# Performance work log

Measured on AMD Instinct MI355X. Metric: run time of the kernel, lower is better.

## Reference

```python
import jax, jax.numpy as jnp
import numpy as np
import math

B = 1048576
BG_RES = 512
NUM_LEVELS = 2
POWER = 4
MIPNOISE = 0.5
INIT_VAL = -2.0


def cube_face_uv(v):
    # v: [N,3] direction vectors. OpenGL cubemap face convention
    # (faces: 0:+x 1:-x 2:+y 3:-y 4:+z 5:-z), as used by nvdiffrast 'cube'.
    x, y, z = v[:, 0], v[:, 1], v[:, 2]
    ax, ay, az = jnp.abs(x), jnp.abs(y), jnp.abs(z)
    is_x = (ax >= ay) & (ax >= az)
    is_y = (~is_x) & (ay >= az)
    face = jnp.where(is_x, jnp.where(x >= 0, 0, 1),
                     jnp.where(is_y, jnp.where(y >= 0, 2, 3),
                               jnp.where(z >= 0, 4, 5))).astype(jnp.int32)
    ma = jnp.where(is_x, ax, jnp.where(is_y, ay, az))
    sc = jnp.where(is_x, jnp.where(x >= 0, -z, z),
                   jnp.where(is_y, x, jnp.where(z >= 0, x, -x)))
    tc = jnp.where(is_x, -y, jnp.where(is_y, jnp.where(y >= 0, z, -z), -y))
    u = 0.5 * (sc / ma + 1.0)
    t = 0.5 * (tc / ma + 1.0)
    return face, u, t


def build_pyramid(tex):
    # tex: [6,R,R,3] -> list of 2x2 box-filtered mips down to 1x1 (nvdiffrast style)
    levels = [tex]
    t = tex
    while t.shape[1] > 1:
        R = t.shape[1]
        t = t.reshape(6, R // 2, 2, R // 2, 2, 3).mean(axis=(2, 4))
        levels.append(t)
    return levels


def bilinear(tex, face, u, v):
    # tex: [6,R,R,3]; face/u/v: [N]. Clamp-to-edge bilinear per selected face.
    R = tex.shape[1]
    x = u * R - 0.5
    y = v * R - 0.5
    x0f = jnp.floor(x); y0f = jnp.floor(y)
    fx = (x - x0f)[:, None]; fy = (y - y0f)[:, None]
    x0 = jnp.clip(x0f.astype(jnp.int32), 0, R - 1)
    y0 = jnp.clip(y0f.astype(jnp.int32), 0, R - 1)
    x1 = jnp.clip(x0f.astype(jnp.int32) + 1, 0, R - 1)
    y1 = jnp.clip(y0f.astype(jnp.int32) + 1, 0, R - 1)
    flat = tex.reshape(6 * R * R, 3)
    base = face * (R * R)
    g00 = flat[base + y0 * R + x0]
    g01 = flat[base + y0 * R + x1]
    g10 = flat[base + y1 * R + x0]
    g11 = flat[base + y1 * R + x1]
    return ((1 - fx) * (1 - fy) * g00 + fx * (1 - fy) * g01 +
            (1 - fx) * fy * g10 + fx * fy * g11)


def sample_cubemap(tex6, face, u, v, mip):
    # trilinear: bilinear in two adjacent mips, lerp by fractional mip level
    levels = build_pyramid(tex6)
    lmax = float(len(levels) - 1)
    m = jnp.clip(mip, 0.0, lmax)
    out = jnp.zeros((face.shape[0], 3), tex6.dtype)
    for l, t in enumerate(levels):
        wl = jnp.clip(1.0 - jnp.abs(m - l), 0.0, 1.0)  # (1-f)/f trilinear weights
        out = out + wl[:, None] * bilinear(t, face, u, v)
    return out


def setup_inputs() -> dict:
    key = jax.random.key(0)
    k1, k2, k3, k4, k5 = jax.random.split(key, 5)
    viewdirs = jax.random.normal(k1, (B, 3), dtype=jnp.float32)
    viewdirs = viewdirs / jnp.linalg.norm(viewdirs, axis=-1, keepdims=True)
    saSample = jax.random.normal(k2, (B,), dtype=jnp.float32)
    noise_u = jax.random.uniform(k3, (B,), dtype=jnp.float32)
    # parameters (init_val*ones/(num_levels-i) in torch; perturbed for nontrivial grads)
    bg_mat0 = (INIT_VAL * jnp.ones((1, 6, 128, 128, 3), jnp.float32)
               + 0.1 * jax.random.normal(k4, (1, 6, 128, 128, 3), jnp.float32))
    bg_mat1 = (INIT_VAL / 2.0 * jnp.ones((1, 6, 512, 512, 3), jnp.float32)
               + 0.1 * jax.random.normal(k5, (1, 6, 512, 512, 3), jnp.float32))
    return {
        "viewdirs": viewdirs,
        "saSample": saSample,
        "noise_u": noise_u,
        "bg_mat0": bg_mat0,
        "bg_mat1": bg_mat1,
        "brightness": jnp.asarray(0.0, jnp.float32),
        "mul": jnp.asarray(1.0, jnp.float32),
        "mipbias": jnp.asarray(0.5, jnp.float32),
    }


def reference(viewdirs, saSample, noise_u, bg_mat0, bg_mat1, brightness, mul, mipbias):
    h = w = BG_RES  # from bg_mats[-1]
    # sa2mip
    distortion = 1.0 / jnp.max(jnp.abs(viewdirs), axis=-1)  # 1/||u||_inf
    saTexel = distortion / h / w
    miplevel = ((saSample - jnp.log(saTexel)) / math.log(POWER) / 2.0
                + mipbias + MIPNOISE * noise_u)
    miplevel = jnp.maximum(miplevel, 0.0)

    face, u, t = cube_face_uv(viewdirs)
    sumemb = sample_cubemap(bg_mat0[0], face, u, t, miplevel)  # mip 1 (128)
    sumemb = sumemb + sample_cubemap(bg_mat1[0], face, u, t, miplevel)  # mip 0 (512)

    # activation == 'identity' branch: exp(x).clip(0.01, 1000)
    img = jnp.clip(jnp.exp(jnp.clip(brightness, -1.0, 2.0) + mul * sumemb), 0.01, 1000.0)
    return img
```

## Files before the change

kernel.cpp:

```cpp
#include <hip/hip_runtime.h>
#include <hip/hip_bf16.h>
#include <math.h>


#define NPYR1_4 524286

__device__ __constant__ int OFFS0[7] = {0, 24576, 30720, 32256, 32640, 32736, 32760};
__device__ __constant__ int OFFS1[9] = {0, 393216, 491520, 516096, 522240,
                                        523776, 524160, 524256, 524280};
static const int H_OFFS0[7] = {0, 24576, 30720, 32256, 32640, 32736, 32760};
static const int H_OFFS1[9] = {0, 393216, 491520, 516096, 522240,
                               523776, 524160, 524256, 524280};

struct PyrArgs {
    const void* src;
    float4* dst[5];
    int R;
    int tpf;
    int T;
    int nlev;
    int rgba;
};

__global__ __launch_bounds__(256) void pyr_kernel(PyrArgs a0, PyrArgs a1, int split) {
    __shared__ float4 A[32 * 32];
    __shared__ float4 Bb[16 * 16];

    PyrArgs a = (blockIdx.x < (unsigned)split) ? a0 : a1;
    int bid = (blockIdx.x < (unsigned)split) ? blockIdx.x : blockIdx.x - split;

    const int tpf = a.tpf;
    const int face = bid / (tpf * tpf);
    const int tif = bid - face * tpf * tpf;
    const int ty = tif / tpf, tx = tif - (tif / tpf) * tpf;
    const int T = a.T, R = a.R;
    const int tid = threadIdx.x;
    const int baseY = ty * T, baseX = tx * T;

    const int total = T * T;
    if (a.rgba) {
        const float4* src = (const float4*)a.src;
        for (int idx = tid; idx < total; idx += 256) {
            int r = idx / T, c = idx - (idx / T) * T;
            A[r * T + c] = src[(size_t)(face * R + baseY + r) * R + baseX + c];
        }
    } else {
        const float* src = (const float*)a.src;
        for (int idx = tid; idx < total; idx += 256) {
            int r = idx / T, c = idx - (idx / T) * T;
            const float* p = src + ((size_t)(face * R + baseY + r) * R + baseX + c) * 3;
            A[r * T + c] = make_float4(p[0], p[1], p[2], 0.f);
        }
    }
    __syncthreads();

    float4* cur = A;
    float4* nxt = Bb;
    int curT = T;
    for (int l = 0; l < a.nlev; ++l) {
        const int nT = curT >> 1;
        const int Rg = R >> (l + 1);
        const int tb = T >> (l + 1);
        float4* dst = a.dst[l];
        const int n = nT * nT;
        for (int idx = tid; idx < n; idx += 256) {
            int ly = idx / nT, lx = idx - (idx / nT) * nT;
            float4 q00 = cur[(2 * ly) * curT + 2 * lx];
            float4 q01 = cur[(2 * ly) * curT + 2 * lx + 1];
            float4 q10 = cur[(2 * ly + 1) * curT + 2 * lx];
            float4 q11 = cur[(2 * ly + 1) * curT + 2 * lx + 1];
            float4 s = make_float4(0.25f * (q00.x + q01.x + q10.x + q11.x),
                                   0.25f * (q00.y + q01.y + q10.y + q11.y),
                                   0.25f * (q00.z + q01.z + q10.z + q11.z), 0.f);
            nxt[ly * nT + lx] = s;
            dst[(size_t)(face * Rg + ty * tb + ly) * Rg + tx * tb + lx] = s;
        }
        __syncthreads();
        float4* tmp = cur; cur = nxt; nxt = tmp;
        curT = nT;
    }
}

__device__ __forceinline__ void bilin4(const float4* __restrict__ tex, int R,
                                       int face, float u, float v, float o[3]) {
    float xf = u * (float)R - 0.5f;
    float yf = v * (float)R - 0.5f;
    float x0f = floorf(xf), y0f = floorf(yf);
    float fx = xf - x0f, fy = yf - y0f;
    int xi = (int)x0f, yi = (int)y0f;
    int x0 = min(max(xi, 0), R - 1);
    int x1 = min(max(xi + 1, 0), R - 1);
    int y0 = min(max(yi, 0), R - 1);
    int y1 = min(max(yi + 1, 0), R - 1);
    const float4* base = tex + (size_t)face * R * R;
    float4 p00 = base[y0 * R + x0];
    float4 p01 = base[y0 * R + x1];
    float4 p10 = base[y1 * R + x0];
    float4 p11 = base[y1 * R + x1];
    float w00 = (1.f - fx) * (1.f - fy);
    float w01 = fx * (1.f - fy);
    float w10 = (1.f - fx) * fy;
    float w11 = fx * fy;
    o[0] = w00 * p00.x + w01 * p01.x + w10 * p10.x + w11 * p11.x;
    o[1] = w00 * p00.y + w01 * p01.y + w10 * p10.y + w11 * p11.y;
    o[2] = w00 * p00.z + w01 * p01.z + w10 * p10.z + w11 * p11.z;
}

__device__ __forceinline__ void bilin3(const float* __restrict__ tex, int R,
                                       int face, float u, float v, float o[3]) {
    float xf = u * (float)R - 0.5f;
    float yf = v * (float)R - 0.5f;
    float x0f = floorf(xf), y0f = floorf(yf);
    float fx = xf - x0f, fy = yf - y0f;
    int xi = (int)x0f, yi = (int)y0f;
    int x0 = min(max(xi, 0), R - 1);
    int x1 = min(max(xi + 1, 0), R - 1);
    int y0 = min(max(yi, 0), R - 1);
    int y1 = min(max(yi + 1, 0), R - 1);
    const float* base = tex + (size_t)face * R * R * 3;
    const float* p00 = base + (y0 * R + x0) * 3;
    const float* p01 = base + (y0 * R + x1) * 3;
    const float* p10 = base + (y1 * R + x0) * 3;
    const float* p11 = base + (y1 * R + x1) * 3;
    float w00 = (1.f - fx) * (1.f - fy);
    float w01 = fx * (1.f - fy);
    float w10 = (1.f - fx) * fy;
    float w11 = fx * fy;
#pragma unroll
    for (int c = 0; c < 3; ++c)
        o[c] = w00 * p00[c] + w01 * p01[c] + w10 * p10[c] + w11 * p11[c];
}

__device__ __forceinline__ void sample_pyr(const float* __restrict__ base_tex,
                                           const float4* __restrict__ pyr,
                                           const int* offs, int lmax, int R0,
                                           int face, float u, float v, float mip,
                                           float o[3]) {
    float m = fminf(fmaxf(mip, 0.f), (float)lmax);
    float l0f = floorf(m);
    int l0 = (int)l0f;
    float f = m - l0f;
    float c0[3];
    if (l0 == 0)
        bilin3(base_tex, R0, face, u, v, c0);
    else
        bilin4(pyr + offs[l0 - 1], R0 >> l0, face, u, v, c0);
    if (f > 0.f && l0 < lmax) {
        float c1[3];
        bilin4(pyr + offs[l0], R0 >> (l0 + 1), face, u, v, c1);
        float w0 = 1.f - f;
#pragma unroll
        for (int c = 0; c < 3; ++c) o[c] = w0 * c0[c] + f * c1[c];
    } else {
#pragma unroll
        for (int c = 0; c < 3; ++c) o[c] = c0[c];
    }
}

__global__ __launch_bounds__(256) void sample_kernel(
    const float* __restrict__ vd, const float* __restrict__ sa,
    const float* __restrict__ nu, const float* __restrict__ tex0,
    const float* __restrict__ tex1, const float* __restrict__ sb,
    const float* __restrict__ sm, const float* __restrict__ smb,
    const float4* __restrict__ pyr0, const float4* __restrict__ pyr1,
    float* __restrict__ out, int n) {
    int i = blockIdx.x * 256 + threadIdx.x;
    if (i >= n) return;

    float x = vd[3 * i + 0];
    float y = vd[3 * i + 1];
    float z = vd[3 * i + 2];
    float ax = fabsf(x), ay = fabsf(y), az = fabsf(z);

    bool is_x = (ax >= ay) && (ax >= az);
    bool is_y = (!is_x) && (ay >= az);

    int face;
    float ma, sc, tc;
    if (is_x) {
        face = (x >= 0.f) ? 0 : 1;
        ma = ax;
        sc = (x >= 0.f) ? -z : z;
        tc = -y;
    } else if (is_y) {
        face = (y >= 0.f) ? 2 : 3;
        ma = ay;
        sc = x;
        tc = (y >= 0.f) ? z : -z;
    } else {
        face = (z >= 0.f) ? 4 : 5;
        ma = az;
        sc = (z >= 0.f) ? x : -x;
        tc = -y;
    }
    float u = 0.5f * (sc / ma + 1.f);
    float t = 0.5f * (tc / ma + 1.f);

    float distortion = 1.f / ma;
    float saTexel = distortion / 512.f / 512.f;
    float mip = (sa[i] - logf(saTexel)) / 1.3862943611198906f / 2.0f +
                smb[0] + 0.5f * nu[i];
    mip = fmaxf(mip, 0.f);

    float s0[3], s1[3];
    sample_pyr(tex0, pyr0, OFFS0, 7, 128, face, u, t, mip, s0);
    sample_pyr(tex1, pyr1, OFFS1, 9, 512, face, u, t, mip, s1);

    float b = fminf(fmaxf(sb[0], -1.f), 2.f);
    float mul = sm[0];
#pragma unroll
    for (int c = 0; c < 3; ++c) {
        float e = expf(b + mul * (s0[c] + s1[c]));
        out[3 * i + c] = fminf(fmaxf(e, 0.01f), 1000.f);
    }
}

extern "C" void kernel_launch(void* const* d_in, const int* in_sizes, int n_in,
                              void* d_out, int out_size, void* d_ws, size_t ws_size,
                              hipStream_t stream) {
    const float* vd = (const float*)d_in[0];
    const float* sa = (const float*)d_in[1];
    const float* nu = (const float*)d_in[2];
    const float* tex0 = (const float*)d_in[3];
    const float* tex1 = (const float*)d_in[4];
    const float* br = (const float*)d_in[5];
    const float* mu = (const float*)d_in[6];
    const float* mb = (const float*)d_in[7];
    float* out = (float*)d_out;

    float4* pyr1 = (float4*)d_ws;
    float4* pyr0 = pyr1 + NPYR1_4;

    const int B = in_sizes[1];

    PyrArgs a0{}, a1{};
    a0.src = tex1; a0.R = 512; a0.tpf = 16; a0.T = 32; a0.nlev = 5; a0.rgba = 0;
    for (int l = 0; l < 5; ++l) a0.dst[l] = pyr1 + H_OFFS1[l];
    a1.src = tex0; a1.R = 128; a1.tpf = 4; a1.T = 32; a1.nlev = 5; a1.rgba = 0;
    for (int l = 0; l < 5; ++l) a1.dst[l] = pyr0 + H_OFFS0[l];
    int split1 = 6 * 16 * 16;
    int grid1 = split1 + 6 * 4 * 4;
    hipLaunchKernelGGL(pyr_kernel, dim3(grid1), dim3(256), 0, stream, a0, a1, split1);

    PyrArgs b0{}, b1{};
    b0.src = pyr1 + H_OFFS1[4]; b0.R = 16; b0.tpf = 1; b0.T = 16; b0.nlev = 4; b0.rgba = 1;
    for (int l = 0; l < 4; ++l) b0.dst[l] = pyr1 + H_OFFS1[5 + l];
    b1.src = pyr0 + H_OFFS0[4]; b1.R = 4; b1.tpf = 1; b1.T = 4; b1.nlev = 2; b1.rgba = 1;
    for (int l = 0; l < 2; ++l) b1.dst[l] = pyr0 + H_OFFS0[5 + l];
    hipLaunchKernelGGL(pyr_kernel, dim3(12), dim3(256), 0, stream, b0, b1, 6);

    int grid = (B + 255) / 256;
    hipLaunchKernelGGL(sample_kernel, dim3(grid), dim3(256), 0, stream,
                       vd, sa, nu, tex0, tex1, br, mu, mb, pyr0, pyr1, out, B);
}
```

Before: 137.4 us.

## Fuse coarse mip levels into sampling kernel via shared-memory pyramid

Removes the second tiny pyramid launch. Each block of a persistent grid-stride sampling kernel (512 blocks) now loads the 16x16 and smaller mip levels into LDS, reduces them to 1x1 there, and samples the coarse levels from LDS instead of global memory. This cuts a serialized launch and global traffic for the coarse taps. The cost is about 64KB of LDS per block, which limits occupancy, plus redundant per-block reduction work.

```diff
diff --git a/kernel.cpp b/kernel.cpp
--- a/kernel.cpp
+++ b/kernel.cpp
@@ -11,6 +11,8 @@
 static const int H_OFFS0[7] = {0, 24576, 30720, 32256, 32640, 32736, 32760};
 static const int H_OFFS1[9] = {0, 393216, 491520, 516096, 522240,
                                523776, 524160, 524256, 524280};
+
+__device__ __constant__ int LOFF[5] = {0, 1536, 1920, 2016, 2040};
 
 struct PyrArgs {
     const void* src;
@@ -19,7 +21,6 @@
     int tpf;
     int T;
     int nlev;
-    int rgba;
 };
 
 __global__ __launch_bounds__(256) void pyr_kernel(PyrArgs a0, PyrArgs a1, int split) {
@@ -38,19 +39,11 @@
     const int baseY = ty * T, baseX = tx * T;
 
     const int total = T * T;
-    if (a.rgba) {
-        const float4* src = (const float4*)a.src;
-        for (int idx = tid; idx < total; idx += 256) {
-            int r = idx / T, c = idx - (idx / T) * T;
-            A[r * T + c] = src[(size_t)(face * R + baseY + r) * R + baseX + c];
-        }
-    } else {
-        const float* src = (const float*)a.src;
-        for (int idx = tid; idx < total; idx += 256) {
-            int r = idx / T, c = idx - (idx / T) * T;
-            const float* p = src + ((size_t)(face * R + baseY + r) * R + baseX + c) * 3;
-            A[r * T + c] = make_float4(p[0], p[1], p[2], 0.f);
-        }
+    const float* src = (const float*)a.src;
+    for (int idx = tid; idx < total; idx += 256) {
+        int r = idx / T, c = idx - (idx / T) * T;
+        const float* p = src + ((size_t)(face * R + baseY + r) * R + baseX + c) * 3;
+        A[r * T + c] = make_float4(p[0], p[1], p[2], 0.f);
     }
     __syncthreads();
 
@@ -81,26 +74,32 @@
     }
 }
 
-__device__ __forceinline__ void bilin4(const float4* __restrict__ tex, int R,
-                                       int face, float u, float v, float o[3]) {
+
+__device__ __forceinline__ void wuv(int R, float u, float v, int& x0, int& x1,
+                                    int& y0, int& y1, float& fx, float& fy) {
     float xf = u * (float)R - 0.5f;
     float yf = v * (float)R - 0.5f;
     float x0f = floorf(xf), y0f = floorf(yf);
-    float fx = xf - x0f, fy = yf - y0f;
+    fx = xf - x0f;
+    fy = yf - y0f;
     int xi = (int)x0f, yi = (int)y0f;
-    int x0 = min(max(xi, 0), R - 1);
-    int x1 = min(max(xi + 1, 0), R - 1);
-    int y0 = min(max(yi, 0), R - 1);
-    int y1 = min(max(yi + 1, 0), R - 1);
+    x0 = min(max(xi, 0), R - 1);
+    x1 = min(max(xi + 1, 0), R - 1);
+    y0 = min(max(yi, 0), R - 1);
+    y1 = min(max(yi + 1, 0), R - 1);
+}
+
+__device__ __forceinline__ void bilin4(const float4* __restrict__ tex, int R,
+                                       int face, float u, float v, float o[3]) {
+    int x0, x1, y0, y1; float fx, fy;
+    wuv(R, u, v, x0, x1, y0, y1, fx, fy);
     const float4* base = tex + (size_t)face * R * R;
     float4 p00 = base[y0 * R + x0];
     float4 p01 = base[y0 * R + x1];
     float4 p10 = base[y1 * R + x0];
     float4 p11 = base[y1 * R + x1];
-    float w00 = (1.f - fx) * (1.f - fy);
-    float w01 = fx * (1.f - fy);
-    float w10 = (1.f - fx) * fy;
-    float w11 = fx * fy;
+    float w00 = (1.f - fx) * (1.f - fy), w01 = fx * (1.f - fy);
+    float w10 = (1.f - fx) * fy, w11 = fx * fy;
     o[0] = w00 * p00.x + w01 * p01.x + w10 * p10.x + w11 * p11.x;
     o[1] = w00 * p00.y + w01 * p01.y + w10 * p10.y + w11 * p11.y;
     o[2] = w00 * p00.z + w01 * p01.z + w10 * p10.z + w11 * p11.z;
@@ -108,52 +107,71 @@
 
 __device__ __forceinline__ void bilin3(const float* __restrict__ tex, int R,
                                        int face, float u, float v, float o[3]) {
-    float xf = u * (float)R - 0.5f;
-    float yf = v * (float)R - 0.5f;
-    float x0f = floorf(xf), y0f = floorf(yf);
-    float fx = xf - x0f, fy = yf - y0f;
-    int xi = (int)x0f, yi = (int)y0f;
-    int x0 = min(max(xi, 0), R - 1);
-    int x1 = min(max(xi + 1, 0), R - 1);
-    int y0 = min(max(yi, 0), R - 1);
-    int y1 = min(max(yi + 1, 0), R - 1);
+    int x0, x1, y0, y1; float fx, fy;
+    wuv(R, u, v, x0, x1, y0, y1, fx, fy);
     const float* base = tex + (size_t)face * R * R * 3;
     const float* p00 = base + (y0 * R + x0) * 3;
     const float* p01 = base + (y0 * R + x1) * 3;
     const float* p10 = base + (y1 * R + x0) * 3;
     const float* p11 = base + (y1 * R + x1) * 3;
-    float w00 = (1.f - fx) * (1.f - fy);
-    float w01 = fx * (1.f - fy);
-    float w10 = (1.f - fx) * fy;
-    float w11 = fx * fy;
+    float w00 = (1.f - fx) * (1.f - fy), w01 = fx * (1.f - fy);
+    float w10 = (1.f - fx) * fy, w11 = fx * fy;
 #pragma unroll
     for (int c = 0; c < 3; ++c)
         o[c] = w00 * p00[c] + w01 * p01[c] + w10 * p10[c] + w11 * p11[c];
 }
 
-__device__ __forceinline__ void sample_pyr(const float* __restrict__ base_tex,
-                                           const float4* __restrict__ pyr,
-                                           const int* offs, int lmax, int R0,
-                                           int face, float u, float v, float mip,
-                                           float o[3]) {
-    float m = fminf(fmaxf(mip, 0.f), (float)lmax);
-    float l0f = floorf(m);
-    int l0 = (int)l0f;
-    float f = m - l0f;
-    float c0[3];
-    if (l0 == 0)
-        bilin3(base_tex, R0, face, u, v, c0);
-    else
-        bilin4(pyr + offs[l0 - 1], R0 >> l0, face, u, v, c0);
-    if (f > 0.f && l0 < lmax) {
-        float c1[3];
-        bilin4(pyr + offs[l0], R0 >> (l0 + 1), face, u, v, c1);
-        float w0 = 1.f - f;
-#pragma unroll
-        for (int c = 0; c < 3; ++c) o[c] = w0 * c0[c] + f * c1[c];
-    } else {
-#pragma unroll
-        for (int c = 0; c < 3; ++c) o[c] = c0[c];
+__device__ __forceinline__ void bilinL(const float4* __restrict__ L, int lb, int R,
+                                       int face, float u, float v, float o[3]) {
+    int x0, x1, y0, y1; float fx, fy;
+    wuv(R, u, v, x0, x1, y0, y1, fx, fy);
+    const float4* base = L + lb + face * R * R;
+    float4 p00 = base[y0 * R + x0];
+    float4 p01 = base[y0 * R + x1];
+    float4 p10 = base[y1 * R + x0];
+    float4 p11 = base[y1 * R + x1];
+    float w00 = (1.f - fx) * (1.f - fy), w01 = fx * (1.f - fy);
+    float w10 = (1.f - fx) * fy, w11 = fx * fy;
+    o[0] = w00 * p00.x + w01 * p01.x + w10 * p10.x + w11 * p11.x;
+    o[1] = w00 * p00.y + w01 * p01.y + w10 * p10.y + w11 * p11.y;
+    o[2] = w00 * p00.z + w01 * p01.z + w10 * p10.z + w11 * p11.z;
+}
+
+__device__ __forceinline__ void tap1(const float4* __restrict__ L,
+                                     const float* __restrict__ tex1,
+                                     const float4* __restrict__ pyr1, int l,
+                                     int face, float u, float v, float o[3]) {
+    if (l >= 5)      bilinL(L, LOFF[l - 5], 16 >> (l - 5), face, u, v, o);
+    else if (l >= 1) bilin4(pyr1 + OFFS1[l - 1], 512 >> l, face, u, v, o);
+    else             bilin3(tex1, 512, face, u, v, o);
+}
+
+__device__ __forceinline__ void tap0(const float4* __restrict__ L,
+                                     const float* __restrict__ tex0,
+                                     const float4* __restrict__ pyr0, int l,
+                                     int face, float u, float v, float o[3]) {
+    if (l >= 3)      bilinL(L, 2046 + LOFF[l - 3], 16 >> (l - 3), face, u, v, o);
+    else if (l >= 1) bilin4(pyr0 + OFFS0[l - 1], 128 >> l, face, u, v, o);
+    else             bilin3(tex0, 128, face, u, v, o);
+}
+
+__device__ __forceinline__ void lds_reduce(float4* L, int sb, int sr, int db,
+                                           int tid) {
+    int dr = sr >> 1;
+    int n = 6 * dr * dr;
+    for (int idx = tid; idx < n; idx += 256) {
+        int f = idx / (dr * dr);
+        int rem = idx - f * dr * dr;
+        int y = rem / dr, x = rem - y * dr;
+        const float4* s = L + sb + f * sr * sr;
+        float4 q00 = s[(2 * y) * sr + 2 * x];
+        float4 q01 = s[(2 * y) * sr + 2 * x + 1];
+        float4 q10 = s[(2 * y + 1) * sr + 2 * x];
+        float4 q11 = s[(2 * y + 1) * sr + 2 * x + 1];
+        L[db + f * dr * dr + y * dr + x] =
+            make_float4(0.25f * (q00.x + q01.x + q10.x + q11.x),
+                        0.25f * (q00.y + q01.y + q10.y + q11.y),
+                        0.25f * (q00.z + q01.z + q10.z + q11.z), 0.f);
     }
 }
 
@@ -164,54 +182,95 @@
     const float* __restrict__ sm, const float* __restrict__ smb,
     const float4* __restrict__ pyr0, const float4* __restrict__ pyr1,
     float* __restrict__ out, int n) {
-    int i = blockIdx.x * 256 + threadIdx.x;
-    if (i >= n) return;
-
-    float x = vd[3 * i + 0];
-    float y = vd[3 * i + 1];
-    float z = vd[3 * i + 2];
-    float ax = fabsf(x), ay = fabsf(y), az = fabsf(z);
-
-    bool is_x = (ax >= ay) && (ax >= az);
-    bool is_y = (!is_x) && (ay >= az);
-
-    int face;
-    float ma, sc, tc;
-    if (is_x) {
-        face = (x >= 0.f) ? 0 : 1;
-        ma = ax;
-        sc = (x >= 0.f) ? -z : z;
-        tc = -y;
-    } else if (is_y) {
-        face = (y >= 0.f) ? 2 : 3;
-        ma = ay;
-        sc = x;
-        tc = (y >= 0.f) ? z : -z;
-    } else {
-        face = (z >= 0.f) ? 4 : 5;
-        ma = az;
-        sc = (z >= 0.f) ? x : -x;
-        tc = -y;
-    }
-    float u = 0.5f * (sc / ma + 1.f);
-    float t = 0.5f * (tc / ma + 1.f);
-
-    float distortion = 1.f / ma;
-    float saTexel = distortion / 512.f / 512.f;
-    float mip = (sa[i] - logf(saTexel)) / 1.3862943611198906f / 2.0f +
-                smb[0] + 0.5f * nu[i];
-    mip = fmaxf(mip, 0.f);
-
-    float s0[3], s1[3];
-    sample_pyr(tex0, pyr0, OFFS0, 7, 128, face, u, t, mip, s0);
-    sample_pyr(tex1, pyr1, OFFS1, 9, 512, face, u, t, mip, s1);
-
-    float b = fminf(fmaxf(sb[0], -1.f), 2.f);
-    float mul = sm[0];
+    __shared__ float4 L[4092];
+    const int tid = threadIdx.x;
+
+    for (int i = tid; i < 1536; i += 256) L[i] = pyr1[OFFS1[4] + i];
+    for (int i = tid; i < 1536; i += 256) L[2046 + i] = pyr0[OFFS0[2] + i];
+    for (int i = tid; i < 384; i += 256)  L[3582 + i] = pyr0[OFFS0[3] + i];
+    for (int i = tid; i < 96; i += 256)   L[3966 + i] = pyr0[OFFS0[4] + i];
+    __syncthreads();
+    lds_reduce(L, 0, 16, 1536, tid);
+    lds_reduce(L, 3966, 4, 4062, tid);
+    __syncthreads();
+    lds_reduce(L, 1536, 8, 1920, tid);
+    lds_reduce(L, 4062, 2, 4086, tid);
+    __syncthreads();
+    lds_reduce(L, 1920, 4, 2016, tid);
+    __syncthreads();
+    lds_reduce(L, 2016, 2, 2040, tid);
+    __syncthreads();
+
+    const float brightness = fminf(fmaxf(sb[0], -1.f), 2.f);
+    const float mul = sm[0];
+    const float mipbias = smb[0];
+
+    const int stride = gridDim.x * 256;
+    for (int i = blockIdx.x * 256 + tid; i < n; i += stride) {
+        float x = vd[3 * i + 0];
+        float y = vd[3 * i + 1];
+        float z = vd[3 * i + 2];
+        float ax = fabsf(x), ay = fabsf(y), az = fabsf(z);
+
+        bool is_x = (ax >= ay) && (ax >= az);
+        bool is_y = (!is_x) && (ay >= az);
+
+        int face;
+        float ma, sc, tc;
+        if (is_x) {
+            face = (x >= 0.f) ? 0 : 1;
+            ma = ax; sc = (x >= 0.f) ? -z : z; tc = -y;
+        } else if (is_y) {
+            face = (y >= 0.f) ? 2 : 3;
+            ma = ay; sc = x; tc = (y >= 0.f) ? z : -z;
+        } else {
+            face = (z >= 0.f) ? 4 : 5;
+            ma = az; sc = (z >= 0.f) ? x : -x; tc = -y;
+        }
+        float u = 0.5f * (sc / ma + 1.f);
+        float t = 0.5f * (tc / ma + 1.f);
+
+        float saTexel = (1.f / ma) / 512.f / 512.f;
+        float mip = (sa[i] - logf(saTexel)) / 1.3862943611198906f / 2.0f +
+                    mipbias + 0.5f * nu[i];
+        mip = fmaxf(mip, 0.f);
+
+        float s0[3];
+        {
+            float m = fminf(mip, 7.f);
+            float l0f = floorf(m);
+            int l0 = (int)l0f;
+            float f = m - l0f;
+            tap0(L, tex0, pyr0, l0, face, u, t, s0);
+            if (f > 0.f && l0 < 7) {
+                float c1[3];
+                tap0(L, tex0, pyr0, l0 + 1, face, u, t, c1);
+                float w0 = 1.f - f;
 #pragma unroll
-    for (int c = 0; c < 3; ++c) {
-        float e = expf(b + mul * (s0[c] + s1[c]));
-        out[3 * i + c] = fminf(fmaxf(e, 0.01f), 1000.f);
+                for (int c = 0; c < 3; ++c) s0[c] = w0 * s0[c] + f * c1[c];
+            }
+        }
+        float s1[3];
+        {
+            float m = fminf(mip, 9.f);
+            float l0f = floorf(m);
+            int l0 = (int)l0f;
+            float f = m - l0f;
+            tap1(L, tex1, pyr1, l0, face, u, t, s1);
+            if (f > 0.f && l0 < 9) {
+                float c1[3];
+                tap1(L, tex1, pyr1, l0 + 1, face, u, t, c1);
+                float w0 = 1.f - f;
+#pragma unroll
+                for (int c = 0; c < 3; ++c) s1[c] = w0 * s1[c] + f * c1[c];
+            }
+        }
+
+#pragma unroll
+        for (int c = 0; c < 3; ++c) {
+            float e = expf(brightness + mul * (s0[c] + s1[c]));
+            out[3 * i + c] = fminf(fmaxf(e, 0.01f), 1000.f);
+        }
     }
 }
 
@@ -234,22 +293,14 @@
     const int B = in_sizes[1];
 
     PyrArgs a0{}, a1{};
-    a0.src = tex1; a0.R = 512; a0.tpf = 16; a0.T = 32; a0.nlev = 5; a0.rgba = 0;
+    a0.src = tex1; a0.R = 512; a0.tpf = 16; a0.T = 32; a0.nlev = 5;
     for (int l = 0; l < 5; ++l) a0.dst[l] = pyr1 + H_OFFS1[l];
-    a1.src = tex0; a1.R = 128; a1.tpf = 4; a1.T = 32; a1.nlev = 5; a1.rgba = 0;
+    a1.src = tex0; a1.R = 128; a1.tpf = 4; a1.T = 32; a1.nlev = 5;
     for (int l = 0; l < 5; ++l) a1.dst[l] = pyr0 + H_OFFS0[l];
     int split1 = 6 * 16 * 16;
     int grid1 = split1 + 6 * 4 * 4;
     hipLaunchKernelGGL(pyr_kernel, dim3(grid1), dim3(256), 0, stream, a0, a1, split1);
 
-    PyrArgs b0{}, b1{};
-    b0.src = pyr1 + H_OFFS1[4]; b0.R = 16; b0.tpf = 1; b0.T = 16; b0.nlev = 4; b0.rgba = 1;
-    for (int l = 0; l < 4; ++l) b0.dst[l] = pyr1 + H_OFFS1[5 + l];
-    b1.src = pyr0 + H_OFFS0[4]; b1.R = 4; b1.tpf = 1; b1.T = 4; b1.nlev = 2; b1.rgba = 1;
-    for (int l = 0; l < 2; ++l) b1.dst[l] = pyr0 + H_OFFS0[5 + l];
-    hipLaunchKernelGGL(pyr_kernel, dim3(12), dim3(256), 0, stream, b0, b1, 6);
-
-    int grid = (B + 255) / 256;
-    hipLaunchKernelGGL(sample_kernel, dim3(grid), dim3(256), 0, stream,
+    hipLaunchKernelGGL(sample_kernel, dim3(512), dim3(256), 0, stream,
                        vd, sa, nu, tex0, tex1, br, mu, mb, pyr0, pyr1, out, B);
 }
```

After: 143.3 us. 1.04x slower.
